# Optimization experiments

Measured on AMD Instinct MI355X. Metric: run time of the kernel, lower is better.

Reference implementation:

```python
import jax, jax.numpy as jnp
import numpy as np

N, T, D = 32, 64, 16
F = 512  # object_classes == feature dim after object_fc


def _gcn(x, adj, W, b):
    # Kipf GraphConvolution: adj @ (x @ W) + b
    return adj @ (x @ W) + b


def _norm_adj(a):
    d = jnp.sum(a, axis=1) ** -0.5
    return a * d[:, None] * d[None, :]


def _per_graph(x, gc1_W, gc1_b, gc2_W, gc2_b, gc3_W, gc3_b, gc4_W, gc4_b):
    # x: [D, F]
    # graph_generator / adj2: softmax-style similarity adjacency with D^{-1/2} norm
    s = x @ x.T                                   # [D, D]
    a = jnp.exp(s - jnp.max(s, axis=1, keepdims=True))
    adj = _norm_adj(a)
    # branch 1
    x1 = jax.nn.relu(_gcn(x, adj, gc1_W, gc1_b))
    x1 = _gcn(x1, adj, gc2_W, gc2_b)
    # branch 2 (adj_hat2 identical construction from x)
    y2 = jax.nn.relu(_gcn(x, adj, gc3_W, gc3_b))  # [D, 32]
    y22 = y2 @ y2.T
    nrm = jnp.sqrt(jnp.sum(y22 * y22, axis=1, keepdims=True))  # torch.norm(y22, 2, dim=1)
    adj3 = 1.0 + y22 / (nrm @ nrm.T)
    adj_hat3 = _norm_adj(adj3)
    y2 = _gcn(y2, adj_hat3, gc4_W, gc4_b)
    return (x1 + y2) * 0.5


def setup_inputs() -> dict:
    key = jax.random.key(0)
    ks = jax.random.split(key, 12)
    s = 0.02
    return {
        "object_raw": jax.random.normal(ks[0], (N * T * D, F), jnp.float32),
        "action_raw": jax.random.normal(ks[1], (N * T, F), jnp.float32),
        "W_obj": jax.random.normal(ks[2], (F, 512), jnp.float32) * s,
        "b_obj": jnp.zeros((512,), jnp.float32),
        "W_act": jax.random.normal(ks[3], (F, 512), jnp.float32) * s,
        "b_act": jnp.zeros((512,), jnp.float32),
        "gc1_W": jax.random.normal(ks[4], (512, 32), jnp.float32) * s,
        "gc1_b": jnp.zeros((32,), jnp.float32),
        "gc2_W": jax.random.normal(ks[5], (32, 512), jnp.float32) * s,
        "gc2_b": jnp.zeros((512,), jnp.float32),
        "gc3_W": jax.random.normal(ks[6], (512, 32), jnp.float32) * s,
        "gc3_b": jnp.zeros((32,), jnp.float32),
        "gc4_W": jax.random.normal(ks[7], (32, 512), jnp.float32) * s,
        "gc4_b": jnp.zeros((512,), jnp.float32),
        "fc1_W": jax.random.normal(ks[8], (512, 1024), jnp.float32) * s,
        "fc1_b": jnp.zeros((1024,), jnp.float32),
        "clf_W": jax.random.normal(ks[9], (1024, 500), jnp.float32) * s,
        "clf_b": jnp.zeros((500,), jnp.float32),
    }


def reference(object_raw, action_raw, W_obj, b_obj, W_act, b_act,
              gc1_W, gc1_b, gc2_W, gc2_b, gc3_W, gc3_b, gc4_W, gc4_b,
              fc1_W, fc1_b, clf_W, clf_b):
    obj = jax.nn.relu(object_raw @ W_obj + b_obj).reshape(N * T, D, 512)
    act = jax.nn.relu(action_raw @ W_act + b_act)           # [N*T, 512]
    obj = obj.at[:, D // 2].set(act)                         # overwrite middle frame
    graph = jax.vmap(lambda x: _per_graph(x, gc1_W, gc1_b, gc2_W, gc2_b,
                                          gc3_W, gc3_b, gc4_W, gc4_b))(obj)
    g = graph.reshape(N, T, D, 512).mean(axis=2)
    o = obj.reshape(N, T, D, 512).mean(axis=2)
    feat = (o + g) * 0.5                                     # graph_fusion == 'mean'
    c = jax.nn.relu(feat)                                    # dropout = identity (eval)
    c = jax.nn.relu(c @ fc1_W + fc1_b)
    out = (c @ clf_W + clf_b).mean(axis=1)                   # mean over T -> [N, 500]
    return out
```

## Files before the change

kernel.cpp:

```cpp
#include <hip/hip_runtime.h>
#include <hip/hip_bf16.h>

using ushort_t = unsigned short;
using f32x4  = __attribute__((ext_vector_type(4))) float;
using short8 = __attribute__((ext_vector_type(8))) short;

__device__ __forceinline__ float bflo(unsigned p) {
    union { unsigned u; float f; } x; x.u = p << 16; return x.f;
}
__device__ __forceinline__ float bfhi(unsigned p) {
    union { unsigned u; float f; } x; x.u = p & 0xffff0000u; return x.f;
}
__device__ __forceinline__ ushort_t f2bf(float f) {
    __hip_bfloat16 h = __float2bfloat16(f);
    return *(ushort_t*)&h;
}
__device__ __forceinline__ unsigned pk2bf(float lo, float hi) {
    __hip_bfloat162 h = __float22bfloat162_rn({lo, hi});
    return *(unsigned*)&h;
}

__device__ __forceinline__ void tr_tile(const float* __restrict__ S, ushort_t* __restrict__ D,
                                        int K, int N, int Npad, int bx, int by,
                                        int tx, int ty, float* tile )
// ... 309 lines not shown
            af[i] = *(const short8*)(AsS + row * 32 + (fq ^ ((fr >> 1) & 3)) * 8);
        }
#pragma unroll
        for (int j = 0; j < 4; j++) {
            const int row = nb + j * 16 + fr;
            bf[j] = *(const short8*)(Bs + row * 32 + (fq ^ ((fr >> 1) & 3)) * 8);
        }
#pragma unroll
        for (int i = 0; i < 4; i++)
#pragma unroll
            for (int j = 0; j < 4; j++)
                acc[i * 4 + j] = __builtin_amdgcn_mfma_f32_16x16x32_bf16(
                    af[i], bf[j], acc[i * 4 + j], 0, 0, 0);
    }

    const int nidx = (bm + mb) >> 6;
#pragma unroll
    for (int j = 0; j < 4; j++) {
        const int n = bn + nb + j * 16 + fr;
        const float bv = bias[n];
        float s = 0.f;
#pragma unroll
        for (int i = 0; i < 4; i++) {
            const f32x4 a = acc[i * 4 + j];
#pragma unroll
            for (int r = 0; r < 4; r++) s += fmaxf(a[r] + bv, 0.f);
        }
        s += __shfl_xor(s, 16);
        s += __shfl_xor(s, 32);
        if (fq == 0) cmean[(size_t)nidx * 1024 + n] = s * (1.0f / 64.0f);
    }
}

__global__ __launch_bounds__(64)
void graph_mfma(const ushort_t* __restrict__ obj,
                const ushort_t* __restrict__ W1t, const float* __restrict__ b1,
                const ushort_t* __restrict__ W2b, const float* __restrict__ b2,
                const ushort_t* __restrict__ W3t, const float* __restrict__ b3,
                const ushort_t* __restrict__ W4b, const float* __restrict__ b4,
                ushort_t* __restrict__ cbuf)
{
    __shared__ float ssb[16 * 17];
    __shared__ float adjt[16 * 20];
    __shared__ float t1s[16 * 36];
    __shared__ float t3s[16 * 36];
    __shared__ float x1s[16 * 36];
    __shared__ float y2s[16 * 36];
    __shared__ float y22s[16 * 17];
    __shared__ float a3t[16 * 20];
    __shared__ float dv[16], dv3[16], nrm[16], cA[16], cA3[16];
    __shared__ float zc1[32], zc4[32];

    const int lane = threadIdx.x;
    const int r = lane & 15, fq = lane >> 4;
    const ushort_t* xg = obj + (size_t)blockIdx.x * 8192;

    short8 xf[16];
#pragma unroll
    for (int kk = 0; kk < 16; kk++)
        xf[kk] = *(const short8*)(xg + r * 512 + kk * 32 + fq * 8);

    f32x4 sacc = (f32x4){0.f, 0.f, 0.f, 0.f};
#pragma unroll
    for (int kk = 0; kk < 16; kk++)
        sacc = __builtin_amdgcn_mfma_f32_16x16x32_bf16(xf[kk], xf[kk], sacc, 0, 0, 0);

    f32x4 a10 = (f32x4){0.f,0.f,0.f,0.f}, a11 = a10, a30 = a10, a31 = a10;
#pragma unroll
    for (int kk = 0; kk < 16; kk++) {
        const short8 w10 = *(const short8*)(W1t + (size_t)(r)      * 512 + kk * 32 + fq * 8);
        const short8 w11 = *(const short8*)(W1t + (size_t)(16 + r) * 512 + kk * 32 + fq * 8);
        const short8 w30 = *(const short8*)(W3t + (size_t)(r)      * 512 + kk * 32 + fq * 8);
        const short8 w31 = *(const short8*)(W3t + (size_t)(16 + r) * 512 + kk * 32 + fq * 8);
        a10 = __builtin_amdgcn_mfma_f32_16x16x32_bf16(xf[kk], w10, a10, 0, 0, 0);
        a11 = __builtin_amdgcn_mfma_f32_16x16x32_bf16(xf[kk], w11, a11, 0, 0, 0);
        a30 = __builtin_amdgcn_mfma_f32_16x16x32_bf16(xf[kk], w30, a30, 0, 0, 0);
        a31 = __builtin_amdgcn_mfma_f32_16x16x32_bf16(xf[kk], w31, a31, 0, 0, 0);
    }

#pragma unroll
    for (int i = 0; i < 4; i++) {
        const int m = fq * 4 + i;
        ssb[m * 17 + r] = sacc[i];
        t1s[m * 36 + r]      = a10[i];
        t1s[m * 36 + 16 + r] = a11[i];
        t3s[m * 36 + r]      = a30[i];
        t3s[m * 36 + 16 + r] = a31[i];
    }
    __syncthreads();

    if (lane < 16) {
        float m = ssb[lane * 17];
#pragma unroll
        for (int j = 1; j < 16; j++) m = fmaxf(m, ssb[lane * 17 + j]);
        float s = 0.f;
#pragma unroll
        for (int j = 0; j < 16; j++) {
            const float e = expf(ssb[lane * 17 + j] - m);
            ssb[lane * 17 + j] = e; s += e;
        }
        dv[lane] = rsqrtf(s);
    }
    __syncthreads();

    {
        const float di = dv[r];
#pragma unroll
        for (int p = 0; p < 4; p++) {
            const int j = fq * 4 + p;
            adjt[j * 20 + r] = ssb[r * 17 + j] * di * dv[j];
        }
    }
    __syncthreads();

    if (lane < 16) {
        float s = 0.f;
#pragma unroll
        for (int i = 0; i < 16; i++) s += adjt[lane * 20 + i];
        cA[lane] = s;
    }

    {
        const int c = lane & 31, hi = lane >> 5;
        const float bb1 = b1[c], bb3 = b3[c];
        float ax[8], ay[8];
#pragma unroll
        for (int i = 0; i < 8; i++) { ax[i] = bb1; ay[i] = bb3; }
#pragma unroll
        for (int j = 0; j < 16; j++) {
            const float t1v = t1s[j * 36 + c], t3v = t3s[j * 36 + c];
            const float4 p = *(const float4*)&adjt[j * 20 + hi * 8];
            const float4 q = *(const float4*)&adjt[j * 20 + hi * 8 + 4];
            ax[0] = fmaf(p.x, t1v, ax[0]); ax[1] = fmaf(p.y, t1v, ax[1]);
            ax[2] = fmaf(p.z, t1v, ax[2]); ax[3] = fmaf(p.w, t1v, ax[3]);
            ax[4] = fmaf(q.x, t1v, ax[4]); ax[5] = fmaf(q.y, t1v, ax[5]);
            ax[6] = fmaf(q.z, t1v, ax[6]); ax[7] = fmaf(q.w, t1v, ax[7]);
            ay[0] = fmaf(p.x, t3v, ay[0]); ay[1] = fmaf(p.y, t3v, ay[1]);
            ay[2] = fmaf(p.z, t3v, ay[2]); ay[3] = fmaf(p.w, t3v, ay[3]);
            ay[4] = fmaf(q.x, t3v, ay[4]); ay[5] = fmaf(q.y, t3v, ay[5]);
            ay[6] = fmaf(q.z, t3v, ay[6]); ay[7] = fmaf(q.w, t3v, ay[7]);
        }
#pragma unroll
        for (int i = 0; i < 8; i++) {
            x1s[(hi * 8 + i) * 36 + c] = fmaxf(ax[i], 0.f);
            y2s[(hi * 8 + i) * 36 + c] = fmaxf(ay[i], 0.f);
        }
    }
    __syncthreads();

    {
        const int i2 = lane >> 2, j0 = (lane & 3) * 4;
        float a4[4] = {0.f, 0.f, 0.f, 0.f};
#pragma unroll
        for (int k4 = 0; k4 < 8; k4++) {
            const float4 yi = *(const float4*)&y2s[i2 * 36 + k4 * 4];
#pragma unroll
            for (int p = 0; p < 4; p++) {
                const float4 yj = *(const float4*)&y2s[(j0 + p) * 36 + k4 * 4];
                a4[p] = fmaf(yi.x, yj.x, a4[p]); a4[p] = fmaf(yi.y, yj.y, a4[p]);
                a4[p] = fmaf(yi.z, yj.z, a4[p]); a4[p] = fmaf(yi.w, yj.w, a4[p]);
            }
        }
#pragma unroll
        for (int p = 0; p < 4; p++) y22s[i2 * 17 + j0 + p] = a4[p];
    }
    __syncthreads();

    if (lane < 16) {
        float sq = 0.f;
#pragma unroll
        for (int j = 0; j < 16; j++) { const float v = y22s[lane * 17 + j]; sq = fmaf(v, v, sq); }
        nrm[lane] = sqrtf(sq);
    }
    __syncthreads();

    {
        const float ni = nrm[r];
#pragma unroll
        for (int p = 0; p < 4; p++) {
            const int j = fq * 4 + p;
            a3t[j * 20 + r] = 1.0f + y22s[r * 17 + j] / (ni * nrm[j]);
        }
    }
    __syncthreads();

    if (lane < 16) {
        float s = 0.f;
#pragma unroll
        for (int j = 0; j < 16; j++) s += a3t[j * 20 + lane];
        dv3[lane] = rsqrtf(s);
    }
    __syncthreads();

    if (lane < 16) {
        float s = 0.f;
#pragma unroll
        for (int i = 0; i < 16; i++) s = fmaf(a3t[lane * 20 + i], dv3[i], s);
        cA3[lane] = s * dv3[lane];
    }
    __syncthreads();

    if (lane < 32) {
        float s1 = 0.f, s4 = 0.f;
#pragma unroll
        for (int j = 0; j < 16; j++) {
            s1 = fmaf(cA[j],  x1s[j * 36 + lane], s1);
            s4 = fmaf(cA3[j], y2s[j * 36 + lane], s4);
        }
        zc1[lane] = s1; zc4[lane] = s4;
    }
    __syncthreads();

    {
        float om[8] = {0,0,0,0,0,0,0,0};
#pragma unroll
        for (int m = 0; m < 16; m++) {
            const uint4 q = *(const uint4*)(xg + m * 512 + lane * 8);
            om[0] += bflo(q.x); om[1] += bfhi(q.x);
            om[2] += bflo(q.y); om[3] += bfhi(q.y);
            om[4] += bflo(q.z); om[5] += bfhi(q.z);
            om[6] += bflo(q.w); om[7] += bfhi(q.w);
        }
        float gm[8] = {0,0,0,0,0,0,0,0};
        for (int k = 0; k < 32; k++) {
            const float z1 = zc1[k], z4 = zc4[k];
            const uint4 w2 = *(const uint4*)(W2b + (size_t)k * 512 + lane * 8);
            const uint4 w4 = *(const uint4*)(W4b + (size_t)k * 512 + lane * 8);
            gm[0] = fmaf(z1, bflo(w2.x), gm[0]); gm[0] = fmaf(z4, bflo(w4.x), gm[0]);
            gm[1] = fmaf(z1, bfhi(w2.x), gm[1]); gm[1] = fmaf(z4, bfhi(w4.x), gm[1]);
            gm[2] = fmaf(z1, bflo(w2.y), gm[2]); gm[2] = fmaf(z4, bflo(w4.y), gm[2]);
            gm[3] = fmaf(z1, bfhi(w2.y), gm[3]); gm[3] = fmaf(z4, bfhi(w4.y), gm[3]);
            gm[4] = fmaf(z1, bflo(w2.z), gm[4]); gm[4] = fmaf(z4, bflo(w4.z), gm[4]);
            gm[5] = fmaf(z1, bfhi(w2.z), gm[5]); gm[5] = fmaf(z4, bfhi(w4.z), gm[5]);
            gm[6] = fmaf(z1, bflo(w2.w), gm[6]); gm[6] = fmaf(z4, bflo(w4.w), gm[6]);
            gm[7] = fmaf(z1, bfhi(w2.w), gm[7]); gm[7] = fmaf(z4, bfhi(w4.w), gm[7]);
        }
        const float4 b2a = *(const float4*)&b2[lane * 8];
        const float4 b2b = *(const float4*)&b2[lane * 8 + 4];
        const float4 b4a = *(const float4*)&b4[lane * 8];
        const float4 b4b = *(const float4*)&b4[lane * 8 + 4];
        const float bs[8] = { b2a.x + b4a.x, b2a.y + b4a.y, b2a.z + b4a.z, b2a.w + b4a.w,
                              b2b.x + b4b.x, b2b.y + b4b.y, b2b.z + b4b.z, b2b.w + b4b.w };
        ushort_t pk[8];
#pragma unroll
        for (int c = 0; c < 8; c++) {
            const float gmean = 0.5f * bs[c] + gm[c] * (1.0f / 32.0f);
            const float feat  = 0.5f * (om[c] * 0.0625f + gmean);
            pk[c] = f2bf(fmaxf(feat, 0.f));
        }
        *(uint4*)(cbuf + (size_t)blockIdx.x * 512 + lane * 8) = *(uint4*)pk;
    }
}

__global__ __launch_bounds__(256)
void clf_col(const float* __restrict__ cmean, const float* __restrict__ Wt,
             const float* __restrict__ clf_b, float* __restrict__ out)
{
    __shared__ float red[8][33];
    const int j = blockIdx.x;
    const int t = threadIdx.x;
    const int n = t & 31, kp = t >> 5;
    const float* cm = cmean + (size_t)n * 1024 + kp * 128;
    const float* wp = Wt + (size_t)j * 1024 + kp * 128;
    float acc = 0.f;
#pragma unroll
    for (int k = 0; k < 128; k += 4) {
        const float4 c = *(const float4*)(cm + k);
        const float4 wv = *(const float4*)(wp + k);
        acc = fmaf(c.x, wv.x, acc);
        acc = fmaf(c.y, wv.y, acc);
        acc = fmaf(c.z, wv.z, acc);
        acc = fmaf(c.w, wv.w, acc);
    }
    red[kp][n] = acc;
    __syncthreads();
    if (t < 32) {
        float s = red[0][t];
#pragma unroll
        for (int p = 1; p < 8; p++) s += red[p][t];
        out[(size_t)t * 500 + j] = s + clf_b[j];
    }
}

// ... 3 lines not shown
{
    const float* object_raw = (const float*)d_in[0];
    const float* action_raw = (const float*)d_in[1];
    const float* W_obj = (const float*)d_in[2];
    const float* b_obj = (const float*)d_in[3];
    const float* W_act = (const float*)d_in[4];
    const float* b_act = (const float*)d_in[5];
    const float* gc1_W = (const float*)d_in[6];
    const float* gc1_b = (const float*)d_in[7];
    const float* gc2_W = (const float*)d_in[8];
    const float* gc2_b = (const float*)d_in[9];
    const float* gc3_W = (const float*)d_in[10];
    const float* gc3_b = (const float*)d_in[11];
    const float* gc4_W = (const float*)d_in[12];
    const float* gc4_b = (const float*)d_in[13];
    const float* fc1_W = (const float*)d_in[14];
    const float* fc1_b = (const float*)d_in[15];
    const float* clf_W = (const float*)d_in[16];
    const float* clf_b = (const float*)d_in[17];

    char* ws = (char*)d_ws;
    const size_t MB = 1024 * 1024;
    ushort_t* obj_bf = (ushort_t*)(ws);
    ushort_t* cbuf   = (ushort_t*)(ws + 32 * MB);
    float*    WclfT  = (float*)   (ws + 34 * MB);
    float*    cmean  = (float*)   (ws + 38 * MB);
    ushort_t* WobjT  = (ushort_t*)(ws + 39 * MB);
    ushort_t* WactT  = (ushort_t*)(ws + 39 * MB + 512 * 1024);
    ushort_t* fc1T   = (ushort_t*)(ws + 40 * MB);
    ushort_t* W1t    = (ushort_t*)(ws + 41 * MB);
    ushort_t* W3t    = (ushort_t*)(ws + 41 * MB + 32 * 1024);
    ushort_t* W2bf   = (ushort_t*)(ws + 41 * MB + 64 * 1024);
    ushort_t* W4bf   = (ushort_t*)(ws + 41 * MB + 96 * 1024);

    prep_weights<<<dim3(1584), 256, 0, stream>>>(
        W_obj, WobjT, W_act, WactT, fc1_W, fc1T,
        gc1_W, W1t, gc3_W, W3t, gc2_W, W2bf, gc4_W, W4bf,
        clf_W, WclfT);

    gemm_obj_stream<<<dim3(256), 512, 0, stream>>>(object_raw, WobjT, b_obj, obj_bf);

    gemm_dma<1, float><<<dim3(4, 16), 256, 0, stream>>>(
        action_raw, WactT, b_act, obj_bf, 512, 512, 512, 16, 8);

    graph_mfma<<<dim3(2048), 64, 0, stream>>>(
        obj_bf, W1t, gc1_b, W2bf, gc2_b, W3t, gc3_b, W4bf, gc4_b, cbuf);

    gemm_fc1_mean<<<dim3(8, 16), 256, 0, stream>>>(cbuf, fc1T, fc1_b, cmean);

    clf_col<<<dim3(500), 256, 0, stream>>>(cmean, WclfT, clf_b, (float*)d_out);
}
```

Baseline: 229.0 us.

## Split per-graph kernel across four wavefronts with role-specialized MFMA and shuffle reductions

The graph kernel moves from one 64-lane wave to four waves per block. Each wave takes one role: the x·xT similarity MFMA, the gc1 projection, the gc3 projection, or the object-mean accumulation. The serial lane<16 reduction phases become 16-lane shuffle reductions spread over all 256 threads, and the final W2/W4 projection is split over four waves with two columns per thread. This aims to cut per-block latency and register pressure, since the x fragments are no longer all held in registers. The cost is redundant x loads across the three MFMA waves, more barriers over more threads, and more shared memory per block.

```diff
diff --git a/kernel.cpp b/kernel.cpp
--- a/kernel.cpp
+++ b/kernel.cpp
@@ -365,7 +365,7 @@
     }
 }
 
-__global__ __launch_bounds__(64)
+__global__ __launch_bounds__(256)
 void graph_mfma(const ushort_t* __restrict__ obj,
                 const ushort_t* __restrict__ W1t, const float* __restrict__ b1,
                 const ushort_t* __restrict__ W2b, const float* __restrict__ b2,
@@ -381,170 +381,57 @@
     __shared__ float y2s[16 * 36];
     __shared__ float y22s[16 * 17];
     __shared__ float a3t[16 * 20];
+    __shared__ __align__(16) float oms[512];
     __shared__ float dv[16], dv3[16], nrm[16], cA[16], cA3[16];
     __shared__ float zc1[32], zc4[32];
 
-    const int lane = threadIdx.x;
+    const int t = threadIdx.x;
+    const int w = t >> 6, lane = t & 63;
     const int r = lane & 15, fq = lane >> 4;
     const ushort_t* xg = obj + (size_t)blockIdx.x * 8192;
 
-    short8 xf[16];
-#pragma unroll
-    for (int kk = 0; kk < 16; kk++)
-        xf[kk] = *(const short8*)(xg + r * 512 + kk * 32 + fq * 8);
-
-    f32x4 sacc = (f32x4){0.f, 0.f, 0.f, 0.f};
-#pragma unroll
-    for (int kk = 0; kk < 16; kk++)
-        sacc = __builtin_amdgcn_mfma_f32_16x16x32_bf16(xf[kk], xf[kk], sacc, 0, 0, 0);
-
-    f32x4 a10 = (f32x4){0.f,0.f,0.f,0.f}, a11 = a10, a30 = a10, a31 = a10;
-#pragma unroll
-    for (int kk = 0; kk < 16; kk++) {
-        const short8 w10 = *(const short8*)(W1t + (size_t)(r)      * 512 + kk * 32 + fq * 8);
-        const short8 w11 = *(const short8*)(W1t + (size_t)(16 + r) * 512 + kk * 32 + fq * 8);
-        const short8 w30 = *(const short8*)(W3t + (size_t)(r)      * 512 + kk * 32 + fq * 8);
-        const short8 w31 = *(const short8*)(W3t + (size_t)(16 + r) * 512 + kk * 32 + fq * 8);
-        a10 = __builtin_amdgcn_mfma_f32_16x16x32_bf16(xf[kk], w10, a10, 0, 0, 0);
-        a11 = __builtin_amdgcn_mfma_f32_16x16x32_bf16(xf[kk], w11, a11, 0, 0, 0);
-        a30 = __builtin_amdgcn_mfma_f32_16x16x32_bf16(xf[kk], w30, a30, 0, 0, 0);
-        a31 = __builtin_amdgcn_mfma_f32_16x16x32_bf16(xf[kk], w31, a31, 0, 0, 0);
-    }
-
-#pragma unroll
-    for (int i = 0; i < 4; i++) {
-        const int m = fq * 4 + i;
-        ssb[m * 17 + r] = sacc[i];
-        t1s[m * 36 + r]      = a10[i];
-        t1s[m * 36 + 16 + r] = a11[i];
-        t3s[m * 36 + r]      = a30[i];
-        t3s[m * 36 + 16 + r] = a31[i];
-    }
-    __syncthreads();
-
-    if (lane < 16) {
-        float m = ssb[lane * 17];
-#pragma unroll
-        for (int j = 1; j < 16; j++) m = fmaxf(m, ssb[lane * 17 + j]);
-        float s = 0.f;
-#pragma unroll
-        for (int j = 0; j < 16; j++) {
-            const float e = expf(ssb[lane * 17 + j] - m);
-            ssb[lane * 17 + j] = e; s += e;
-        }
-        dv[lane] = rsqrtf(s);
-    }
-    __syncthreads();
-
-    {
-        const float di = dv[r];
-#pragma unroll
-        for (int p = 0; p < 4; p++) {
-            const int j = fq * 4 + p;
-            adjt[j * 20 + r] = ssb[r * 17 + j] * di * dv[j];
-        }
-    }
-    __syncthreads();
-
-    if (lane < 16) {
-        float s = 0.f;
-#pragma unroll
-        for (int i = 0; i < 16; i++) s += adjt[lane * 20 + i];
-        cA[lane] = s;
-    }
-
-    {
-        const int c = lane & 31, hi = lane >> 5;
-        const float bb1 = b1[c], bb3 = b3[c];
-        float ax[8], ay[8];
-#pragma unroll
-        for (int i = 0; i < 8; i++) { ax[i] = bb1; ay[i] = bb3; }
-#pragma unroll
-        for (int j = 0; j < 16; j++) {
-            const float t1v = t1s[j * 36 + c], t3v = t3s[j * 36 + c];
-            const float4 p = *(const float4*)&adjt[j * 20 + hi * 8];
-            const float4 q = *(const float4*)&adjt[j * 20 + hi * 8 + 4];
-            ax[0] = fmaf(p.x, t1v, ax[0]); ax[1] = fmaf(p.y, t1v, ax[1]);
-            ax[2] = fmaf(p.z, t1v, ax[2]); ax[3] = fmaf(p.w, t1v, ax[3]);
-            ax[4] = fmaf(q.x, t1v, ax[4]); ax[5] = fmaf(q.y, t1v, ax[5]);
-            ax[6] = fmaf(q.z, t1v, ax[6]); ax[7] = fmaf(q.w, t1v, ax[7]);
-            ay[0] = fmaf(p.x, t3v, ay[0]); ay[1] = fmaf(p.y, t3v, ay[1]);
-            ay[2] = fmaf(p.z, t3v, ay[2]); ay[3] = fmaf(p.w, t3v, ay[3]);
-            ay[4] = fmaf(q.x, t3v, ay[4]); ay[5] = fmaf(q.y, t3v, ay[5]);
-            ay[6] = fmaf(q.z, t3v, ay[6]); ay[7] = fmaf(q.w, t3v, ay[7]);
-        }
-#pragma unroll
-        for (int i = 0; i < 8; i++) {
-            x1s[(hi * 8 + i) * 36 + c] = fmaxf(ax[i], 0.f);
-            y2s[(hi * 8 + i) * 36 + c] = fmaxf(ay[i], 0.f);
-        }
-    }
-    __syncthreads();
-
-    {
-        const int i2 = lane >> 2, j0 = (lane & 3) * 4;
-        float a4[4] = {0.f, 0.f, 0.f, 0.f};
-#pragma unroll
-        for (int k4 = 0; k4 < 8; k4++) {
-            const float4 yi = *(const float4*)&y2s[i2 * 36 + k4 * 4];
-#pragma unroll
-            for (int p = 0; p < 4; p++) {
-                const float4 yj = *(const float4*)&y2s[(j0 + p) * 36 + k4 * 4];
-                a4[p] = fmaf(yi.x, yj.x, a4[p]); a4[p] = fmaf(yi.y, yj.y, a4[p]);
-                a4[p] = fmaf(yi.z, yj.z, a4[p]); a4[p] = fmaf(yi.w, yj.w, a4[p]);
-            }
-        }
-#pragma unroll
-        for (int p = 0; p < 4; p++) y22s[i2 * 17 + j0 + p] = a4[p];
-    }
-    __syncthreads();
-
-    if (lane < 16) {
-        float sq = 0.f;
-#pragma unroll
-        for (int j = 0; j < 16; j++) { const float v = y22s[lane * 17 + j]; sq = fmaf(v, v, sq); }
-        nrm[lane] = sqrtf(sq);
-    }
-    __syncthreads();
-
-    {
-        const float ni = nrm[r];
-#pragma unroll
-        for (int p = 0; p < 4; p++) {
-            const int j = fq * 4 + p;
-            a3t[j * 20 + r] = 1.0f + y22s[r * 17 + j] / (ni * nrm[j]);
-        }
-    }
-    __syncthreads();
-
-    if (lane < 16) {
-        float s = 0.f;
-#pragma unroll
-        for (int j = 0; j < 16; j++) s += a3t[j * 20 + lane];
-        dv3[lane] = rsqrtf(s);
-    }
-    __syncthreads();
-
-    if (lane < 16) {
-        float s = 0.f;
-#pragma unroll
-        for (int i = 0; i < 16; i++) s = fmaf(a3t[lane * 20 + i], dv3[i], s);
-        cA3[lane] = s * dv3[lane];
-    }
-    __syncthreads();
-
-    if (lane < 32) {
-        float s1 = 0.f, s4 = 0.f;
-#pragma unroll
-        for (int j = 0; j < 16; j++) {
-            s1 = fmaf(cA[j],  x1s[j * 36 + lane], s1);
-            s4 = fmaf(cA3[j], y2s[j * 36 + lane], s4);
-        }
-        zc1[lane] = s1; zc4[lane] = s4;
-    }
-    __syncthreads();
-
-    {
+    if (w == 0) {
+        f32x4 sacc = (f32x4){0.f, 0.f, 0.f, 0.f};
+#pragma unroll 8
+        for (int kk = 0; kk < 16; kk++) {
+            const short8 xk = *(const short8*)(xg + r * 512 + kk * 32 + fq * 8);
+            sacc = __builtin_amdgcn_mfma_f32_16x16x32_bf16(xk, xk, sacc, 0, 0, 0);
+        }
+#pragma unroll
+        for (int i = 0; i < 4; i++) ssb[(fq * 4 + i) * 17 + r] = sacc[i];
+    } else if (w == 1) {
+        f32x4 a10 = (f32x4){0.f,0.f,0.f,0.f}, a11 = a10;
+#pragma unroll 4
+        for (int kk = 0; kk < 16; kk++) {
+            const short8 xk  = *(const short8*)(xg + r * 512 + kk * 32 + fq * 8);
+            const short8 w10 = *(const short8*)(W1t + (size_t)(r)      * 512 + kk * 32 + fq * 8);
+            const short8 w11 = *(const short8*)(W1t + (size_t)(16 + r) * 512 + kk * 32 + fq * 8);
+            a10 = __builtin_amdgcn_mfma_f32_16x16x32_bf16(xk, w10, a10, 0, 0, 0);
+            a11 = __builtin_amdgcn_mfma_f32_16x16x32_bf16(xk, w11, a11, 0, 0, 0);
+        }
+#pragma unroll
+        for (int i = 0; i < 4; i++) {
+            const int m = fq * 4 + i;
+            t1s[m * 36 + r]      = a10[i];
+            t1s[m * 36 + 16 + r] = a11[i];
+        }
+    } else if (w == 2) {
+        f32x4 a30 = (f32x4){0.f,0.f,0.f,0.f}, a31 = a30;
+#pragma unroll 4
+        for (int kk = 0; kk < 16; kk++) {
+            const short8 xk  = *(const short8*)(xg + r * 512 + kk * 32 + fq * 8);
+            const short8 w30 = *(const short8*)(W3t + (size_t)(r)      * 512 + kk * 32 + fq * 8);
+            const short8 w31 = *(const short8*)(W3t + (size_t)(16 + r) * 512 + kk * 32 + fq * 8);
+            a30 = __builtin_amdgcn_mfma_f32_16x16x32_bf16(xk, w30, a30, 0, 0, 0);
+            a31 = __builtin_amdgcn_mfma_f32_16x16x32_bf16(xk, w31, a31, 0, 0, 0);
+        }
+#pragma unroll
+        for (int i = 0; i < 4; i++) {
+            const int m = fq * 4 + i;
+            t3s[m * 36 + r]      = a30[i];
+            t3s[m * 36 + 16 + r] = a31[i];
+        }
+    } else {
         float om[8] = {0,0,0,0,0,0,0,0};
 #pragma unroll
         for (int m = 0; m < 16; m++) {
@@ -554,34 +441,124 @@
             om[4] += bflo(q.z); om[5] += bfhi(q.z);
             om[6] += bflo(q.w); om[7] += bfhi(q.w);
         }
-        float gm[8] = {0,0,0,0,0,0,0,0};
+        *(float4*)&oms[lane * 8]     = (float4){om[0], om[1], om[2], om[3]};
+        *(float4*)&oms[lane * 8 + 4] = (float4){om[4], om[5], om[6], om[7]};
+    }
+    __syncthreads();
+
+    {
+        const int row = t >> 4, col = t & 15;
+        const float v = ssb[row * 17 + col];
+        float mx = v;
+        mx = fmaxf(mx, __shfl_xor(mx, 1));
+        mx = fmaxf(mx, __shfl_xor(mx, 2));
+        mx = fmaxf(mx, __shfl_xor(mx, 4));
+        mx = fmaxf(mx, __shfl_xor(mx, 8));
+        const float e = expf(v - mx);
+        float s = e;
+        s += __shfl_xor(s, 1); s += __shfl_xor(s, 2);
+        s += __shfl_xor(s, 4); s += __shfl_xor(s, 8);
+        ssb[row * 17 + col] = e;
+        if (col == 0) dv[row] = rsqrtf(s);
+    }
+    __syncthreads();
+
+    {
+        const int j = t >> 4, rr = t & 15;
+        const float av = ssb[rr * 17 + j] * dv[rr] * dv[j];
+        adjt[j * 20 + rr] = av;
+        float s = av;
+        s += __shfl_xor(s, 1); s += __shfl_xor(s, 2);
+        s += __shfl_xor(s, 4); s += __shfl_xor(s, 8);
+        if (rr == 0) cA[j] = s;
+    }
+    __syncthreads();
+
+    {
+        const int c = t & 31, g = t >> 5;
+        const int m0 = g * 2, m1 = m0 + 1;
+        const float bb1 = b1[c], bb3 = b3[c];
+        float ax0 = bb1, ax1 = bb1, ay0 = bb3, ay1 = bb3;
+#pragma unroll
+        for (int j = 0; j < 16; j++) {
+            const float t1v = t1s[j * 36 + c], t3v = t3s[j * 36 + c];
+            const float a0 = adjt[j * 20 + m0], a1 = adjt[j * 20 + m1];
+            ax0 = fmaf(a0, t1v, ax0); ax1 = fmaf(a1, t1v, ax1);
+            ay0 = fmaf(a0, t3v, ay0); ay1 = fmaf(a1, t3v, ay1);
+        }
+        x1s[m0 * 36 + c] = fmaxf(ax0, 0.f); x1s[m1 * 36 + c] = fmaxf(ax1, 0.f);
+        y2s[m0 * 36 + c] = fmaxf(ay0, 0.f); y2s[m1 * 36 + c] = fmaxf(ay1, 0.f);
+    }
+    __syncthreads();
+
+    {
+        const int i2 = t >> 4, j2 = t & 15;
+        float s = 0.f;
+#pragma unroll
+        for (int k4 = 0; k4 < 8; k4++) {
+            const float4 yi = *(const float4*)&y2s[i2 * 36 + k4 * 4];
+            const float4 yj = *(const float4*)&y2s[j2 * 36 + k4 * 4];
+            s = fmaf(yi.x, yj.x, s); s = fmaf(yi.y, yj.y, s);
+            s = fmaf(yi.z, yj.z, s); s = fmaf(yi.w, yj.w, s);
+        }
+        y22s[i2 * 17 + j2] = s;
+        float sq = s * s;
+        sq += __shfl_xor(sq, 1); sq += __shfl_xor(sq, 2);
+        sq += __shfl_xor(sq, 4); sq += __shfl_xor(sq, 8);
+        if (j2 == 0) nrm[i2] = sqrtf(sq);
+    }
+    __syncthreads();
+
+    {
+        const int j = t >> 4, rr = t & 15;
+        const float av = 1.0f + y22s[rr * 17 + j] / (nrm[rr] * nrm[j]);
+        a3t[j * 20 + rr] = av;
+        float s = av;
+        s += __shfl_xor(s, 1); s += __shfl_xor(s, 2);
+        s += __shfl_xor(s, 4); s += __shfl_xor(s, 8);
+        if (rr == 0) dv3[j] = rsqrtf(s);
+    }
+    __syncthreads();
+
+    {
+        const int a = t >> 4, b = t & 15;
+        float s = a3t[a * 20 + b] * dv3[b];
+        s += __shfl_xor(s, 1); s += __shfl_xor(s, 2);
+        s += __shfl_xor(s, 4); s += __shfl_xor(s, 8);
+        if (b == 0) cA3[a] = s * dv3[a];
+    }
+    __syncthreads();
+
+    if (t < 32) {
+        float s1 = 0.f, s4 = 0.f;
+#pragma unroll
+        for (int j = 0; j < 16; j++) {
+            s1 = fmaf(cA[j],  x1s[j * 36 + t], s1);
+            s4 = fmaf(cA3[j], y2s[j * 36 + t], s4);
+        }
+        zc1[t] = s1; zc4[t] = s4;
+    }
+    __syncthreads();
+
+    {
+        const int c0 = w * 128 + lane * 2;
+        float gm0 = 0.f, gm1 = 0.f;
+#pragma unroll 8
         for (int k = 0; k < 32; k++) {
             const float z1 = zc1[k], z4 = zc4[k];
-            const uint4 w2 = *(const uint4*)(W2b + (size_t)k * 512 + lane * 8);
-            const uint4 w4 = *(const uint4*)(W4b + (size_t)k * 512 + lane * 8);
-            gm[0] = fmaf(z1, bflo(w2.x), gm[0]); gm[0] = fmaf(z4, bflo(w4.x), gm[0]);
-            gm[1] = fmaf(z1, bfhi(w2.x), gm[1]); gm[1] = fmaf(z4, bfhi(w4.x), gm[1]);
-            gm[2] = fmaf(z1, bflo(w2.y), gm[2]); gm[2] = fmaf(z4, bflo(w4.y), gm[2]);
-            gm[3] = fmaf(z1, bfhi(w2.y), gm[3]); gm[3] = fmaf(z4, bfhi(w4.y), gm[3]);
-            gm[4] = fmaf(z1, bflo(w2.z), gm[4]); gm[4] = fmaf(z4, bflo(w4.z), gm[4]);
-            gm[5] = fmaf(z1, bfhi(w2.z), gm[5]); gm[5] = fmaf(z4, bfhi(w4.z), gm[5]);
-            gm[6] = fmaf(z1, bflo(w2.w), gm[6]); gm[6] = fmaf(z4, bflo(w4.w), gm[6]);
-            gm[7] = fmaf(z1, bfhi(w2.w), gm[7]); gm[7] = fmaf(z4, bfhi(w4.w), gm[7]);
-        }
-        const float4 b2a = *(const float4*)&b2[lane * 8];
-        const float4 b2b = *(const float4*)&b2[lane * 8 + 4];
-        const float4 b4a = *(const float4*)&b4[lane * 8];
-        const float4 b4b = *(const float4*)&b4[lane * 8 + 4];
-        const float bs[8] = { b2a.x + b4a.x, b2a.y + b4a.y, b2a.z + b4a.z, b2a.w + b4a.w,
-                              b2b.x + b4b.x, b2b.y + b4b.y, b2b.z + b4b.z, b2b.w + b4b.w };
-        ushort_t pk[8];
-#pragma unroll
-        for (int c = 0; c < 8; c++) {
-            const float gmean = 0.5f * bs[c] + gm[c] * (1.0f / 32.0f);
-            const float feat  = 0.5f * (om[c] * 0.0625f + gmean);
-            pk[c] = f2bf(fmaxf(feat, 0.f));
-        }
-        *(uint4*)(cbuf + (size_t)blockIdx.x * 512 + lane * 8) = *(uint4*)pk;
+            const unsigned u2 = *(const unsigned*)(W2b + (size_t)k * 512 + c0);
+            const unsigned u4 = *(const unsigned*)(W4b + (size_t)k * 512 + c0);
+            gm0 = fmaf(z1, bflo(u2), gm0); gm0 = fmaf(z4, bflo(u4), gm0);
+            gm1 = fmaf(z1, bfhi(u2), gm1); gm1 = fmaf(z4, bfhi(u4), gm1);
+        }
+        const float bs0 = b2[c0] + b4[c0];
+        const float bs1 = b2[c0 + 1] + b4[c0 + 1];
+        const float gmean0 = 0.5f * bs0 + gm0 * (1.0f / 32.0f);
+        const float gmean1 = 0.5f * bs1 + gm1 * (1.0f / 32.0f);
+        const float f0 = 0.5f * (oms[c0]     * 0.0625f + gmean0);
+        const float f1 = 0.5f * (oms[c0 + 1] * 0.0625f + gmean1);
+        *(unsigned*)(cbuf + (size_t)blockIdx.x * 512 + c0) =
+            pk2bf(fmaxf(f0, 0.f), fmaxf(f1, 0.f));
     }
 }
 
@@ -662,7 +639,7 @@
     gemm_dma<1, float><<<dim3(4, 16), 256, 0, stream>>>(
         action_raw, WactT, b_act, obj_bf, 512, 512, 512, 16, 8);
 
-    graph_mfma<<<dim3(2048), 64, 0, stream>>>(
+    graph_mfma<<<dim3(2048), 256, 0, stream>>>(
         obj_bf, W1t, gc1_b, W2bf, gc2_b, W3t, gc3_b, W4bf, gc4_b, cbuf);
 
     gemm_fc1_mean<<<dim3(8, 16), 256, 0, stream>>>(cbuf, fc1T, fc1_b, cmean);
```

New measurement: 236.3 us. 3.2% more time.

## Split graph kernel into MFMA pre-pass and shuffle-based finishing kernel

Applied to the files above, without the earlier changes.

The per-graph kernel is split in two. graph_pre stages four graphs per 256-thread block in swizzled LDS and gives the X@W1/W3, X·Xᵀ and object-mean work to different waves. graph_fin reads these intermediates from global memory and does the adjacency, normalisation and reductions with wave shuffles instead of serial single-lane loops. The aim is to raise occupancy and parallelism and to shorten the sync-heavy serial sections. In exchange it adds an extra launch and a global round trip for the intermediates, roughly 10 MB of fp32 data.

```diff
diff --git a/kernel.cpp b/kernel.cpp
--- a/kernel.cpp
+++ b/kernel.cpp
@@ -365,223 +365,301 @@
     }
 }
 
+__global__ __launch_bounds__(256)
+void graph_pre(const ushort_t* __restrict__ obj,
+               const ushort_t* __restrict__ W1t, const ushort_t* __restrict__ W3t,
+               float* __restrict__ Sg, float* __restrict__ t1g,
+               float* __restrict__ t3g, float* __restrict__ omsg)
+{
+    __shared__ __align__(16) ushort_t Xs[64 * 512];
+    const int t = threadIdx.x;
+    const int lane = t & 63, w = t >> 6;
+    const int bm = blockIdx.x * 64;
+    const int g0 = blockIdx.x * 4;
+    const int fr = lane & 15, fq = lane >> 4;
+
+#pragma unroll
+    for (int i = 0; i < 16; i++) {
+        const int flat = i * 256 + t;
+        const int row = flat >> 6, c = flat & 63;
+        const uint4 v = *(const uint4*)(obj + (size_t)(bm + row) * 512 + c * 8);
+        *(uint4*)&Xs[row * 512 + ((c ^ (row & 7)) * 8)] = v;
+    }
+    __syncthreads();
+
+    if (w == 1 || w == 2) {
+        const ushort_t* Wt = (w == 1) ? W1t : W3t;
+        float* outp       = (w == 1) ? t1g : t3g;
+        f32x4 a0[4], a1[4];
+#pragma unroll
+        for (int g = 0; g < 4; g++) { a0[g] = (f32x4){0.f,0.f,0.f,0.f}; a1[g] = a0[g]; }
+        for (int kk = 0; kk < 16; kk++) {
+            const short8 wa = *(const short8*)(Wt + (size_t)fr * 512 + kk * 32 + fq * 8);
+            const short8 wb = *(const short8*)(Wt + (size_t)(16 + fr) * 512 + kk * 32 + fq * 8);
+#pragma unroll
+            for (int g = 0; g < 4; g++) {
+                const short8 af = *(const short8*)&Xs[(g * 16 + fr) * 512 + (((kk * 4 + fq) ^ (fr & 7)) * 8)];
+                a0[g] = __builtin_amdgcn_mfma_f32_16x16x32_bf16(af, wa, a0[g], 0, 0, 0);
+                a1[g] = __builtin_amdgcn_mfma_f32_16x16x32_bf16(af, wb, a1[g], 0, 0, 0);
+            }
+        }
+#pragma unroll
+        for (int g = 0; g < 4; g++) {
+#pragma unroll
+            for (int i = 0; i < 4; i++) {
+                const int m = fq * 4 + i;
+                outp[(size_t)(g0 + g) * 512 + m * 32 + fr]      = a0[g][i];
+                outp[(size_t)(g0 + g) * 512 + m * 32 + 16 + fr] = a1[g][i];
+            }
+        }
+    } else {
+        const int gb = (w == 0) ? 0 : 2;
+        f32x4 s0 = (f32x4){0.f,0.f,0.f,0.f}, s1 = s0;
+        for (int kk = 0; kk < 16; kk++) {
+            const short8 af0 = *(const short8*)&Xs[(gb * 16 + fr) * 512 + (((kk * 4 + fq) ^ (fr & 7)) * 8)];
+            const short8 af1 = *(const short8*)&Xs[((gb + 1) * 16 + fr) * 512 + (((kk * 4 + fq) ^ (fr & 7)) * 8)];
+            s0 = __builtin_amdgcn_mfma_f32_16x16x32_bf16(af0, af0, s0, 0, 0, 0);
+            s1 = __builtin_amdgcn_mfma_f32_16x16x32_bf16(af1, af1, s1, 0, 0, 0);
+        }
+#pragma unroll
+        for (int i = 0; i < 4; i++) {
+            const int m = fq * 4 + i;
+            Sg[(size_t)(g0 + gb) * 256 + m * 16 + fr]     = s0[i];
+            Sg[(size_t)(g0 + gb + 1) * 256 + m * 16 + fr] = s1[i];
+        }
+#pragma unroll
+        for (int gg = 0; gg < 2; gg++) {
+            const int g = gb + gg;
+            float om[8] = {0,0,0,0,0,0,0,0};
+#pragma unroll
+            for (int m = 0; m < 16; m++) {
+                const uint4 q = *(const uint4*)&Xs[(g * 16 + m) * 512 + ((lane ^ (m & 7)) * 8)];
+                om[0] += bflo(q.x); om[1] += bfhi(q.x);
+                om[2] += bflo(q.y); om[3] += bfhi(q.y);
+                om[4] += bflo(q.z); om[5] += bfhi(q.z);
+                om[6] += bflo(q.w); om[7] += bfhi(q.w);
+            }
+            *(float4*)(omsg + (size_t)(g0 + g) * 512 + lane * 8)     = (float4){om[0], om[1], om[2], om[3]};
+            *(float4*)(omsg + (size_t)(g0 + g) * 512 + lane * 8 + 4) = (float4){om[4], om[5], om[6], om[7]};
+        }
+    }
+}
+
 __global__ __launch_bounds__(64)
-void graph_mfma(const ushort_t* __restrict__ obj,
-                const ushort_t* __restrict__ W1t, const float* __restrict__ b1,
-                const ushort_t* __restrict__ W2b, const float* __restrict__ b2,
-                const ushort_t* __restrict__ W3t, const float* __restrict__ b3,
-                const ushort_t* __restrict__ W4b, const float* __restrict__ b4,
-                ushort_t* __restrict__ cbuf)
-{
-    __shared__ float ssb[16 * 17];
-    __shared__ float adjt[16 * 20];
-    __shared__ float t1s[16 * 36];
-    __shared__ float t3s[16 * 36];
-    __shared__ float x1s[16 * 36];
-    __shared__ float y2s[16 * 36];
-    __shared__ float y22s[16 * 17];
-    __shared__ float a3t[16 * 20];
-    __shared__ float dv[16], dv3[16], nrm[16], cA[16], cA3[16];
-    __shared__ float zc1[32], zc4[32];
+void graph_fin(const float* __restrict__ Sg, const float* __restrict__ t1g,
+               const float* __restrict__ t3g, const float* __restrict__ omsg,
+               const float* __restrict__ b1, const float* __restrict__ b3,
+               const ushort_t* __restrict__ W2b, const float* __restrict__ b2,
+               const ushort_t* __restrict__ W4b, const float* __restrict__ b4,
+               ushort_t* __restrict__ cbuf)
+{
+    __shared__ float t1S[16 * 36], t3S[16 * 36], y2S[16 * 36];
+    __shared__ float adjS[16 * 17];
+    __shared__ float dvS[16], cAS[16], nrmS[16], dv3S[16], cA3S[16];
+    __shared__ float zc1S[32], zc4S[32];
 
     const int lane = threadIdx.x;
-    const int r = lane & 15, fq = lane >> 4;
-    const ushort_t* xg = obj + (size_t)blockIdx.x * 8192;
-
-    short8 xf[16];
-#pragma unroll
-    for (int kk = 0; kk < 16; kk++)
-        xf[kk] = *(const short8*)(xg + r * 512 + kk * 32 + fq * 8);
-
-    f32x4 sacc = (f32x4){0.f, 0.f, 0.f, 0.f};
-#pragma unroll
-    for (int kk = 0; kk < 16; kk++)
-        sacc = __builtin_amdgcn_mfma_f32_16x16x32_bf16(xf[kk], xf[kk], sacc, 0, 0, 0);
-
-    f32x4 a10 = (f32x4){0.f,0.f,0.f,0.f}, a11 = a10, a30 = a10, a31 = a10;
-#pragma unroll
-    for (int kk = 0; kk < 16; kk++) {
-        const short8 w10 = *(const short8*)(W1t + (size_t)(r)      * 512 + kk * 32 + fq * 8);
-        const short8 w11 = *(const short8*)(W1t + (size_t)(16 + r) * 512 + kk * 32 + fq * 8);
-        const short8 w30 = *(const short8*)(W3t + (size_t)(r)      * 512 + kk * 32 + fq * 8);
-        const short8 w31 = *(const short8*)(W3t + (size_t)(16 + r) * 512 + kk * 32 + fq * 8);
-        a10 = __builtin_amdgcn_mfma_f32_16x16x32_bf16(xf[kk], w10, a10, 0, 0, 0);
-        a11 = __builtin_amdgcn_mfma_f32_16x16x32_bf16(xf[kk], w11, a11, 0, 0, 0);
-        a30 = __builtin_amdgcn_mfma_f32_16x16x32_bf16(xf[kk], w30, a30, 0, 0, 0);
-        a31 = __builtin_amdgcn_mfma_f32_16x16x32_bf16(xf[kk], w31, a31, 0, 0, 0);
-    }
-
-#pragma unroll
-    for (int i = 0; i < 4; i++) {
-        const int m = fq * 4 + i;
-        ssb[m * 17 + r] = sacc[i];
-        t1s[m * 36 + r]      = a10[i];
-        t1s[m * 36 + 16 + r] = a11[i];
-        t3s[m * 36 + r]      = a30[i];
-        t3s[m * 36 + 16 + r] = a31[i];
-    }
-    __syncthreads();
-
-    if (lane < 16) {
-        float m = ssb[lane * 17];
-#pragma unroll
-        for (int j = 1; j < 16; j++) m = fmaxf(m, ssb[lane * 17 + j]);
-        float s = 0.f;
-#pragma unroll
-        for (int j = 0; j < 16; j++) {
-            const float e = expf(ssb[lane * 17 + j] - m);
-            ssb[lane * 17 + j] = e; s += e;
-        }
-        dv[lane] = rsqrtf(s);
-    }
-    __syncthreads();
-
-    {
-        const float di = dv[r];
-#pragma unroll
-        for (int p = 0; p < 4; p++) {
-            const int j = fq * 4 + p;
-            adjt[j * 20 + r] = ssb[r * 17 + j] * di * dv[j];
-        }
-    }
-    __syncthreads();
-
-    if (lane < 16) {
-        float s = 0.f;
-#pragma unroll
-        for (int i = 0; i < 16; i++) s += adjt[lane * 20 + i];
-        cA[lane] = s;
-    }
-
-    {
-        const int c = lane & 31, hi = lane >> 5;
-        const float bb1 = b1[c], bb3 = b3[c];
-        float ax[8], ay[8];
-#pragma unroll
-        for (int i = 0; i < 8; i++) { ax[i] = bb1; ay[i] = bb3; }
-#pragma unroll
-        for (int j = 0; j < 16; j++) {
-            const float t1v = t1s[j * 36 + c], t3v = t3s[j * 36 + c];
-            const float4 p = *(const float4*)&adjt[j * 20 + hi * 8];
-            const float4 q = *(const float4*)&adjt[j * 20 + hi * 8 + 4];
-            ax[0] = fmaf(p.x, t1v, ax[0]); ax[1] = fmaf(p.y, t1v, ax[1]);
-            ax[2] = fmaf(p.z, t1v, ax[2]); ax[3] = fmaf(p.w, t1v, ax[3]);
-            ax[4] = fmaf(q.x, t1v, ax[4]); ax[5] = fmaf(q.y, t1v, ax[5]);
-            ax[6] = fmaf(q.z, t1v, ax[6]); ax[7] = fmaf(q.w, t1v, ax[7]);
-            ay[0] = fmaf(p.x, t3v, ay[0]); ay[1] = fmaf(p.y, t3v, ay[1]);
-            ay[2] = fmaf(p.z, t3v, ay[2]); ay[3] = fmaf(p.w, t3v, ay[3]);
-            ay[4] = fmaf(q.x, t3v, ay[4]); ay[5] = fmaf(q.y, t3v, ay[5]);
-            ay[6] = fmaf(q.z, t3v, ay[6]); ay[7] = fmaf(q.w, t3v, ay[7]);
-        }
-#pragma unroll
-        for (int i = 0; i < 8; i++) {
-            x1s[(hi * 8 + i) * 36 + c] = fmaxf(ax[i], 0.f);
-            y2s[(hi * 8 + i) * 36 + c] = fmaxf(ay[i], 0.f);
-        }
-    }
-    __syncthreads();
-
-    {
-        const int i2 = lane >> 2, j0 = (lane & 3) * 4;
-        float a4[4] = {0.f, 0.f, 0.f, 0.f};
-#pragma unroll
-        for (int k4 = 0; k4 < 8; k4++) {
-            const float4 yi = *(const float4*)&y2s[i2 * 36 + k4 * 4];
-#pragma unroll
-            for (int p = 0; p < 4; p++) {
-                const float4 yj = *(const float4*)&y2s[(j0 + p) * 36 + k4 * 4];
-                a4[p] = fmaf(yi.x, yj.x, a4[p]); a4[p] = fmaf(yi.y, yj.y, a4[p]);
-                a4[p] = fmaf(yi.z, yj.z, a4[p]); a4[p] = fmaf(yi.w, yj.w, a4[p]);
-            }
-        }
-#pragma unroll
-        for (int p = 0; p < 4; p++) y22s[i2 * 17 + j0 + p] = a4[p];
-    }
-    __syncthreads();
-
-    if (lane < 16) {
+    const int r = lane & 15, q = lane >> 4;
+    const int g = blockIdx.x;
+
+    {
+        const int row = lane >> 2, cb = (lane & 3) * 8;
+        const float4 a0 = *(const float4*)(t1g + (size_t)g * 512 + lane * 8);
+        const float4 a1 = *(const float4*)(t1g + (size_t)g * 512 + lane * 8 + 4);
+        const float4 c0v = *(const float4*)(t3g + (size_t)g * 512 + lane * 8);
+        const float4 c1v = *(const float4*)(t3g + (size_t)g * 512 + lane * 8 + 4);
+        *(float4*)&t1S[row * 36 + cb]     = a0;
+        *(float4*)&t1S[row * 36 + cb + 4] = a1;
+        *(float4*)&t3S[row * 36 + cb]     = c0v;
+        *(float4*)&t3S[row * 36 + cb + 4] = c1v;
+    }
+
+    const float4 sv = *(const float4*)(Sg + (size_t)g * 256 + r * 16 + q * 4);
+    float mx = fmaxf(fmaxf(sv.x, sv.y), fmaxf(sv.z, sv.w));
+    mx = fmaxf(mx, __shfl_xor(mx, 16));
+    mx = fmaxf(mx, __shfl_xor(mx, 32));
+    const float e0 = expf(sv.x - mx), e1 = expf(sv.y - mx);
+    const float e2 = expf(sv.z - mx), e3 = expf(sv.w - mx);
+    float rs = e0 + e1 + e2 + e3;
+    rs += __shfl_xor(rs, 16); rs += __shfl_xor(rs, 32);
+    const float dv = rsqrtf(rs);
+    if (q == 0) dvS[r] = dv;
+    __syncthreads();
+
+    float ad0, ad1, ad2, ad3;
+    {
+        const float4 dc = *(const float4*)&dvS[q * 4];
+        ad0 = e0 * dv * dc.x; ad1 = e1 * dv * dc.y;
+        ad2 = e2 * dv * dc.z; ad3 = e3 * dv * dc.w;
+    }
+    adjS[r * 17 + q * 4 + 0] = ad0; adjS[r * 17 + q * 4 + 1] = ad1;
+    adjS[r * 17 + q * 4 + 2] = ad2; adjS[r * 17 + q * 4 + 3] = ad3;
+    {
+        float c0s = ad0, c1s = ad1, c2s = ad2, c3s = ad3;
+#pragma unroll
+        for (int m = 1; m <= 8; m <<= 1) {
+            c0s += __shfl_xor(c0s, m); c1s += __shfl_xor(c1s, m);
+            c2s += __shfl_xor(c2s, m); c3s += __shfl_xor(c3s, m);
+        }
+        if (r == 0) {
+            cAS[q * 4 + 0] = c0s; cAS[q * 4 + 1] = c1s;
+            cAS[q * 4 + 2] = c2s; cAS[q * 4 + 3] = c3s;
+        }
+    }
+    __syncthreads();
+
+    const int c0 = q * 8;
+    float x1v[8], y2v[8];
+    {
+        const float4 b1a = *(const float4*)(b1 + c0);
+        const float4 b1b = *(const float4*)(b1 + c0 + 4);
+        const float4 b3a = *(const float4*)(b3 + c0);
+        const float4 b3b = *(const float4*)(b3 + c0 + 4);
+        x1v[0]=b1a.x; x1v[1]=b1a.y; x1v[2]=b1a.z; x1v[3]=b1a.w;
+        x1v[4]=b1b.x; x1v[5]=b1b.y; x1v[6]=b1b.z; x1v[7]=b1b.w;
+        y2v[0]=b3a.x; y2v[1]=b3a.y; y2v[2]=b3a.z; y2v[3]=b3a.w;
+        y2v[4]=b3b.x; y2v[5]=b3b.y; y2v[6]=b3b.z; y2v[7]=b3b.w;
+    }
+#pragma unroll
+    for (int j = 0; j < 16; j++) {
+        const float a = adjS[r * 17 + j];
+        const float4 t1a = *(const float4*)&t1S[j * 36 + c0];
+        const float4 t1b = *(const float4*)&t1S[j * 36 + c0 + 4];
+        const float4 t3a = *(const float4*)&t3S[j * 36 + c0];
+        const float4 t3b = *(const float4*)&t3S[j * 36 + c0 + 4];
+        x1v[0] = fmaf(a, t1a.x, x1v[0]); x1v[1] = fmaf(a, t1a.y, x1v[1]);
+        x1v[2] = fmaf(a, t1a.z, x1v[2]); x1v[3] = fmaf(a, t1a.w, x1v[3]);
+        x1v[4] = fmaf(a, t1b.x, x1v[4]); x1v[5] = fmaf(a, t1b.y, x1v[5]);
+        x1v[6] = fmaf(a, t1b.z, x1v[6]); x1v[7] = fmaf(a, t1b.w, x1v[7]);
+        y2v[0] = fmaf(a, t3a.x, y2v[0]); y2v[1] = fmaf(a, t3a.y, y2v[1]);
+        y2v[2] = fmaf(a, t3a.z, y2v[2]); y2v[3] = fmaf(a, t3a.w, y2v[3]);
+        y2v[4] = fmaf(a, t3b.x, y2v[4]); y2v[5] = fmaf(a, t3b.y, y2v[5]);
+        y2v[6] = fmaf(a, t3b.z, y2v[6]); y2v[7] = fmaf(a, t3b.w, y2v[7]);
+    }
+#pragma unroll
+    for (int cc = 0; cc < 8; cc++) {
+        x1v[cc] = fmaxf(x1v[cc], 0.f);
+        y2v[cc] = fmaxf(y2v[cc], 0.f);
+        y2S[r * 36 + c0 + cc] = y2v[cc];
+    }
+    __syncthreads();
+
+    float yy[4] = {0.f, 0.f, 0.f, 0.f};
+#pragma unroll
+    for (int k4 = 0; k4 < 8; k4++) {
+        const float4 yi = *(const float4*)&y2S[r * 36 + k4 * 4];
+#pragma unroll
+        for (int i = 0; i < 4; i++) {
+            const float4 yj = *(const float4*)&y2S[(q * 4 + i) * 36 + k4 * 4];
+            yy[i] = fmaf(yi.x, yj.x, yy[i]); yy[i] = fmaf(yi.y, yj.y, yy[i]);
+            yy[i] = fmaf(yi.z, yj.z, yy[i]); yy[i] = fmaf(yi.w, yj.w, yy[i]);
+        }
+    }
+    {
         float sq = 0.f;
 #pragma unroll
-        for (int j = 0; j < 16; j++) { const float v = y22s[lane * 17 + j]; sq = fmaf(v, v, sq); }
-        nrm[lane] = sqrtf(sq);
-    }
-    __syncthreads();
-
-    {
-        const float ni = nrm[r];
-#pragma unroll
-        for (int p = 0; p < 4; p++) {
-            const int j = fq * 4 + p;
-            a3t[j * 20 + r] = 1.0f + y22s[r * 17 + j] / (ni * nrm[j]);
-        }
-    }
-    __syncthreads();
-
-    if (lane < 16) {
-        float s = 0.f;
-#pragma unroll
-        for (int j = 0; j < 16; j++) s += a3t[j * 20 + lane];
-        dv3[lane] = rsqrtf(s);
-    }
-    __syncthreads();
-
-    if (lane < 16) {
-        float s = 0.f;
-#pragma unroll
-        for (int i = 0; i < 16; i++) s = fmaf(a3t[lane * 20 + i], dv3[i], s);
-        cA3[lane] = s * dv3[lane];
-    }
-    __syncthreads();
-
-    if (lane < 32) {
-        float s1 = 0.f, s4 = 0.f;
-#pragma unroll
-        for (int j = 0; j < 16; j++) {
-            s1 = fmaf(cA[j],  x1s[j * 36 + lane], s1);
-            s4 = fmaf(cA3[j], y2s[j * 36 + lane], s4);
-        }
-        zc1[lane] = s1; zc4[lane] = s4;
-    }
-    __syncthreads();
-
-    {
-        float om[8] = {0,0,0,0,0,0,0,0};
-#pragma unroll
-        for (int m = 0; m < 16; m++) {
-            const uint4 q = *(const uint4*)(xg + m * 512 + lane * 8);
-            om[0] += bflo(q.x); om[1] += bfhi(q.x);
-            om[2] += bflo(q.y); om[3] += bfhi(q.y);
-            om[4] += bflo(q.z); om[5] += bfhi(q.z);
-            om[6] += bflo(q.w); om[7] += bfhi(q.w);
-        }
+        for (int i = 0; i < 4; i++) sq = fmaf(yy[i], yy[i], sq);
+        sq += __shfl_xor(sq, 16); sq += __shfl_xor(sq, 32);
+        const float nr = sqrtf(sq);
+        if (q == 0) nrmS[r] = nr;
+    }
+    __syncthreads();
+
+    float a3[4];
+    float dv3;
+    {
+        const float nr = nrmS[r];
+        const float4 ncv = *(const float4*)&nrmS[q * 4];
+        a3[0] = 1.0f + yy[0] / (nr * ncv.x);
+        a3[1] = 1.0f + yy[1] / (nr * ncv.y);
+        a3[2] = 1.0f + yy[2] / (nr * ncv.z);
+        a3[3] = 1.0f + yy[3] / (nr * ncv.w);
+        float d3 = a3[0] + a3[1] + a3[2] + a3[3];
+        d3 += __shfl_xor(d3, 16); d3 += __shfl_xor(d3, 32);
+        dv3 = rsqrtf(d3);
+        if (q == 0) dv3S[r] = dv3;
+    }
+    {
+        const float cAm = cAS[r];
+        float zp[8];
+#pragma unroll
+        for (int cc = 0; cc < 8; cc++) zp[cc] = cAm * x1v[cc];
+#pragma unroll
+        for (int m = 1; m <= 8; m <<= 1)
+#pragma unroll
+            for (int cc = 0; cc < 8; cc++) zp[cc] += __shfl_xor(zp[cc], m);
+        if (r == 0)
+#pragma unroll
+            for (int cc = 0; cc < 8; cc++) zc1S[c0 + cc] = zp[cc];
+    }
+    __syncthreads();
+
+    {
+        const float4 d3c = *(const float4*)&dv3S[q * 4];
+        float p0 = a3[0] * dv3 * d3c.x, p1 = a3[1] * dv3 * d3c.y;
+        float p2 = a3[2] * dv3 * d3c.z, p3 = a3[3] * dv3 * d3c.w;
+#pragma unroll
+        for (int m = 1; m <= 8; m <<= 1) {
+            p0 += __shfl_xor(p0, m); p1 += __shfl_xor(p1, m);
+            p2 += __shfl_xor(p2, m); p3 += __shfl_xor(p3, m);
+        }
+        if (r == 0) {
+            cA3S[q * 4 + 0] = p0; cA3S[q * 4 + 1] = p1;
+            cA3S[q * 4 + 2] = p2; cA3S[q * 4 + 3] = p3;
+        }
+    }
+    __syncthreads();
+
+    {
+        const float cA3m = cA3S[r];
+        float zp[8];
+#pragma unroll
+        for (int cc = 0; cc < 8; cc++) zp[cc] = cA3m * y2v[cc];
+#pragma unroll
+        for (int m = 1; m <= 8; m <<= 1)
+#pragma unroll
+            for (int cc = 0; cc < 8; cc++) zp[cc] += __shfl_xor(zp[cc], m);
+        if (r == 0)
+#pragma unroll
+            for (int cc = 0; cc < 8; cc++) zc4S[c0 + cc] = zp[cc];
+    }
+    __syncthreads();
+
+    {
         float gm[8] = {0,0,0,0,0,0,0,0};
+        const ushort_t* w2p = W2b + lane * 8;
+        const ushort_t* w4p = W4b + lane * 8;
+#pragma unroll 8
         for (int k = 0; k < 32; k++) {
-            const float z1 = zc1[k], z4 = zc4[k];
-            const uint4 w2 = *(const uint4*)(W2b + (size_t)k * 512 + lane * 8);
-            const uint4 w4 = *(const uint4*)(W4b + (size_t)k * 512 + lane * 8);
-            gm[0] = fmaf(z1, bflo(w2.x), gm[0]); gm[0] = fmaf(z4, bflo(w4.x), gm[0]);
-            gm[1] = fmaf(z1, bfhi(w2.x), gm[1]); gm[1] = fmaf(z4, bfhi(w4.x), gm[1]);
-            gm[2] = fmaf(z1, bflo(w2.y), gm[2]); gm[2] = fmaf(z4, bflo(w4.y), gm[2]);
-            gm[3] = fmaf(z1, bfhi(w2.y), gm[3]); gm[3] = fmaf(z4, bfhi(w4.y), gm[3]);
-            gm[4] = fmaf(z1, bflo(w2.z), gm[4]); gm[4] = fmaf(z4, bflo(w4.z), gm[4]);
-            gm[5] = fmaf(z1, bfhi(w2.z), gm[5]); gm[5] = fmaf(z4, bfhi(w4.z), gm[5]);
-            gm[6] = fmaf(z1, bflo(w2.w), gm[6]); gm[6] = fmaf(z4, bflo(w4.w), gm[6]);
-            gm[7] = fmaf(z1, bfhi(w2.w), gm[7]); gm[7] = fmaf(z4, bfhi(w4.w), gm[7]);
-        }
-        const float4 b2a = *(const float4*)&b2[lane * 8];
-        const float4 b2b = *(const float4*)&b2[lane * 8 + 4];
-        const float4 b4a = *(const float4*)&b4[lane * 8];
-        const float4 b4b = *(const float4*)&b4[lane * 8 + 4];
+            const float z1 = zc1S[k], z4 = zc4S[k];
+            const uint4 u2 = *(const uint4*)(w2p + (size_t)k * 512);
+            const uint4 u4 = *(const uint4*)(w4p + (size_t)k * 512);
+            gm[0] = fmaf(z1, bflo(u2.x), gm[0]); gm[0] = fmaf(z4, bflo(u4.x), gm[0]);
+            gm[1] = fmaf(z1, bfhi(u2.x), gm[1]); gm[1] = fmaf(z4, bfhi(u4.x), gm[1]);
+            gm[2] = fmaf(z1, bflo(u2.y), gm[2]); gm[2] = fmaf(z4, bflo(u4.y), gm[2]);
+            gm[3] = fmaf(z1, bfhi(u2.y), gm[3]); gm[3] = fmaf(z4, bfhi(u4.y), gm[3]);
+            gm[4] = fmaf(z1, bflo(u2.z), gm[4]); gm[4] = fmaf(z4, bflo(u4.z), gm[4]);
+            gm[5] = fmaf(z1, bfhi(u2.z), gm[5]); gm[5] = fmaf(z4, bfhi(u4.z), gm[5]);
+            gm[6] = fmaf(z1, bflo(u2.w), gm[6]); gm[6] = fmaf(z4, bflo(u4.w), gm[6]);
+            gm[7] = fmaf(z1, bfhi(u2.w), gm[7]); gm[7] = fmaf(z4, bfhi(u4.w), gm[7]);
+        }
+        const float4 oma = *(const float4*)(omsg + (size_t)g * 512 + lane * 8);
+        const float4 omb = *(const float4*)(omsg + (size_t)g * 512 + lane * 8 + 4);
+        const float om[8] = {oma.x, oma.y, oma.z, oma.w, omb.x, omb.y, omb.z, omb.w};
+        const float4 b2a = *(const float4*)(b2 + lane * 8);
+        const float4 b2b = *(const float4*)(b2 + lane * 8 + 4);
+        const float4 b4a = *(const float4*)(b4 + lane * 8);
+        const float4 b4b = *(const float4*)(b4 + lane * 8 + 4);
         const float bs[8] = { b2a.x + b4a.x, b2a.y + b4a.y, b2a.z + b4a.z, b2a.w + b4a.w,
                               b2b.x + b4b.x, b2b.y + b4b.y, b2b.z + b4b.z, b2b.w + b4b.w };
         ushort_t pk[8];
 #pragma unroll
-        for (int c = 0; c < 8; c++) {
-            const float gmean = 0.5f * bs[c] + gm[c] * (1.0f / 32.0f);
-            const float feat  = 0.5f * (om[c] * 0.0625f + gmean);
-            pk[c] = f2bf(fmaxf(feat, 0.f));
-        }
-        *(uint4*)(cbuf + (size_t)blockIdx.x * 512 + lane * 8) = *(uint4*)pk;
+        for (int cc = 0; cc < 8; cc++) {
+            const float gmean = 0.5f * bs[cc] + gm[cc] * (1.0f / 32.0f);
+            const float feat  = 0.5f * (om[cc] * 0.0625f + gmean);
+            pk[cc] = f2bf(fmaxf(feat, 0.f));
+        }
+        *(uint4*)(cbuf + (size_t)g * 512 + lane * 8) = *(uint4*)pk;
     }
 }
 
@@ -651,6 +729,10 @@
     ushort_t* W3t    = (ushort_t*)(ws + 41 * MB + 32 * 1024);
     ushort_t* W2bf   = (ushort_t*)(ws + 41 * MB + 64 * 1024);
     ushort_t* W4bf   = (ushort_t*)(ws + 41 * MB + 96 * 1024);
+    float*    t1g    = (float*)   (ws + 44 * MB);
+    float*    t3g    = (float*)   (ws + 48 * MB);
+    float*    Sg     = (float*)   (ws + 52 * MB);
+    float*    omsg   = (float*)   (ws + 54 * MB);
 
     prep_weights<<<dim3(1584), 256, 0, stream>>>(
         W_obj, WobjT, W_act, WactT, fc1_W, fc1T,
@@ -662,8 +744,11 @@
     gemm_dma<1, float><<<dim3(4, 16), 256, 0, stream>>>(
         action_raw, WactT, b_act, obj_bf, 512, 512, 512, 16, 8);
 
-    graph_mfma<<<dim3(2048), 64, 0, stream>>>(
-        obj_bf, W1t, gc1_b, W2bf, gc2_b, W3t, gc3_b, W4bf, gc4_b, cbuf);
+    graph_pre<<<dim3(512), 256, 0, stream>>>(
+        obj_bf, W1t, W3t, Sg, t1g, t3g, omsg);
+
+    graph_fin<<<dim3(2048), 64, 0, stream>>>(
+        Sg, t1g, t3g, omsg, gc1_b, gc3_b, W2bf, gc2_b, W4bf, gc4_b, cbuf);
 
     gemm_fc1_mean<<<dim3(8, 16), 256, 0, stream>>>(cbuf, fc1T, fc1_b, cmean);
 
```

New measurement: 230.0 us. About the same (+0.4%).
